# Optimization experiments

Hardware: AMD Instinct MI355X
Metric: run time of the kernel (lower is better)

## Reference

```python
import jax, jax.numpy as jnp
import numpy as np

B, L, DIN, D, H, NL, DFF = 4, 1024, 64, 512, 8, 3, 2048
DH = D // H
N_RBF = 8
LARGE_NEG, CLAMP = 10000.0, 20.0


def layernorm(x, g, b, eps=1e-5):
    m = x.mean(-1, keepdims=True)
    v = x.var(-1, keepdims=True)
    return (x - m) * jax.lax.rsqrt(v + eps) * g + b


def sinusoidal_pe(length, d):
    pos = np.arange(length, dtype=np.float32)[:, None]
    div = np.exp(np.arange(0, d, 2, dtype=np.float32) * (-np.log(10000.0) / d))
    pe = np.zeros((length, d), dtype=np.float32)
    pe[:, 0::2] = np.sin(pos * div)
    pe[:, 1::2] = np.cos(pos * div)
    return jnp.asarray(pe)


def rbf(v):
    centers = jnp.linspace(0.0, 1.0, N_RBF)
    widths = jnp.full((N_RBF,), 0.2)
    diff = (v[..., None] - centers) / (widths + 1e-6)
    return jnp.exp(-0.5 * diff * diff)


def setup_inputs() -> dict:
    key = jax.random.key(0)
    ks = jax.random.split(key, 40)
    g = lambda k, shape: (jax.random.normal(k, shape) * 0.02).astype(jnp.float32)
    feat_dim = D + 2 + 2 * N_RBF  # base PE + raw(2) + 2 RBFs
    inp = {
        "x": jax.random.normal(ks[0], (B, L, DIN), jnp.float32),
        "lengths": jax.random.randint(ks[1], (B,), L // 2, L + 1),
        "input_delay": jax.random.uniform(ks[2], (B,), jnp.float32),
        "c_local": jax.random.uniform(ks[3], (B, L), jnp.float32).at[:, 0].set(0.0),
        "c_sink": jax.random.uniform(ks[4], (B, L), jnp.float32),
        # input projection
        "in_w": g(ks[5], (D, DIN)), "in_b": jnp.zeros((D,)),
        # delay encoder: Linear(1,D) -> GELU -> Linear(D,D) -> LN
        "de_w1": g(ks[6], (D, 1)), "de_b1": jnp.zeros((D,)),
        "de_w2": g(ks[7], (D, D)), "de_b2": jnp.zeros((D,)),
        "de_ln_g": jnp.ones((D,)), "de_ln_b": jnp.zeros((D,)),
        # corr positional encoding
        "cpe_w": g(ks[8], (D, feat_dim)), "cpe_b": jnp.zeros((D,)),
        "cpe_ln_g": jnp.ones((D,)), "cpe_ln_b": jnp.zeros((D,)),
        "gain": jnp.float32(0.5),
        # bias params
        "alpha": jnp.float32(10.0), "beta": jnp.float32(10.0),
        "floor": jnp.float32(0.1), "gamma": jnp.float32(0.7),
        # per-layer stacks
        "inproj_w": g(ks[9], (NL, 3 * D, D)), "inproj_b": jnp.zeros((NL, 3 * D)),
        "outproj_w": g(ks[10], (NL, D, D)), "outproj_b": jnp.zeros((NL, D)),
        "ln1_g": jnp.ones((NL, D)), "ln1_b": jnp.zeros((NL, D)),
        "ln2_g": jnp.ones((NL, D)), "ln2_b": jnp.zeros((NL, D)),
        "ff_w1": g(ks[11], (NL, DFF, D)), "ff_b1": jnp.zeros((NL, DFF)),
        "ff_w2": g(ks[12], (NL, D, DFF)), "ff_b2": jnp.zeros((NL, D)),
        "out_ln_g": jnp.ones((D,)), "out_ln_b": jnp.zeros((D,)),
    }
    return inp


def _forward(x, input_delay, c_local, c_sink, in_w, in_b, de_w1, de_b1, de_w2, de_b2,
             de_ln_g, de_ln_b, cpe_w, cpe_b, cpe_ln_g, cpe_ln_b, gain, alpha, beta,
             floor, gamma, inproj_w, inproj_b, outproj_w, outproj_b, ln1_g, ln1_b,
             ln2_g, ln2_b, ff_w1, ff_b1, ff_w2, ff_b2, out_ln_g, out_ln_b, lengths):
    Bc, Lc, _ = x.shape
    mask = jnp.arange(Lc)[None, :] >= lengths[:, None]          # [B,L] True=pad

    # input projection
    h = x @ in_w.T + in_b

    # delay feature encoder
    e = input_delay[:, None] @ de_w1.T + de_b1
    e = jax.nn.gelu(e, approximate=False) @ de_w2.T + de_b2
    e = layernorm(e, de_ln_g, de_ln_b)
    h = h + e[:, None, :]

    # corr positional encoding (uses clamped correlations)
    cl = jnp.clip(c_local, 0.0, 1.0)
    cs = jnp.clip(c_sink, 0.0, 1.0)
    pe_base = jnp.broadcast_to(sinusoidal_pe(Lc, D)[None], (Bc, Lc, D))
    z = jnp.concatenate([pe_base, jnp.stack([cl, cs], -1), rbf(cl), rbf(cs)], axis=-1)
    pe = layernorm(z @ cpe_w.T + cpe_b, cpe_ln_g, cpe_ln_b)
    pe = gain * pe
    pe = jnp.where(mask[..., None], 0.0, pe)
    h = h + pe

    # neighbor-correlation attention bias [B,1,L,L] (identical across layers/heads)
    idx = jnp.arange(Lc)
    neigh = jnp.abs(idx[None, :] - idx[:, None]) == 1           # [L,L]
    c_edge = jnp.zeros((Bc, Lc, Lc), x.dtype)
    c_edge = c_edge.at[:, 1:, :-1].set(jnp.broadcast_to(c_local[:, 1:, None], (Bc, Lc - 1, Lc - 1)))
    c_edge = c_edge.at[:, :-1, 1:].set(jnp.broadcast_to(c_local[:, None, 1:], (Bc, Lc - 1, Lc - 1)))
    bias = alpha * jnp.where(neigh[None], c_edge, 0.0)
    bias = jnp.where(mask[:, :, None] | mask[:, None, :], 0.0, bias)

    # sink bias (row 0 only): floor + (1-floor)*(c_sink^gamma)
    c_remap = floor + (1.0 - floor) * jnp.power(cs + 1e-6, gamma)
    sink_row = beta * jnp.where(mask, 0.0, c_remap)             # [B,L]
    attn_bias = bias[:, None].at[:, :, 0, :].add(sink_row[:, None, :])  # [B,1,L,L]

    pad = mask[:, None, None, :].astype(x.dtype)                # [B,1,1,L]
    scale = 1.0 / (DH ** 0.5)

    for i in range(NL):
        hn = layernorm(h, ln1_g[i], ln1_b[i])
        qkv = hn @ inproj_w[i].T + inproj_b[i]                  # [B,L,3D]
        q, k, v = jnp.split(qkv, 3, axis=-1)
        q = q.reshape(Bc, Lc, H, DH).transpose(0, 2, 1, 3)      # [B,H,L,d]
        k = k.reshape(Bc, Lc, H, DH).transpose(0, 2, 1, 3)
        v = v.reshape(Bc, Lc, H, DH).transpose(0, 2, 1, 3)
        scores = jnp.einsum('bhqd,bhkd->bhqk', q, k) * scale + attn_bias
        scores = scores - LARGE_NEG * pad
        scores = scores - scores.max(axis=-1, keepdims=True)
        scores = jnp.clip(scores, -CLAMP, CLAMP)
        attn = jax.nn.softmax(scores, axis=-1)
        o = jnp.einsum('bhqk,bhkd->bhqd', attn, v)
        o = o.transpose(0, 2, 1, 3).reshape(Bc, Lc, D)
        h = h + (o @ outproj_w[i].T + outproj_b[i])
        hn2 = layernorm(h, ln2_g[i], ln2_b[i])
        ff = jax.nn.gelu(hn2 @ ff_w1[i].T + ff_b1[i], approximate=False)
        h = h + (ff @ ff_w2[i].T + ff_b2[i])

    return layernorm(h, out_ln_g, out_ln_b)


def reference(x, lengths, input_delay, c_local, c_sink, in_w, in_b, de_w1, de_b1,
              de_w2, de_b2, de_ln_g, de_ln_b, cpe_w, cpe_b, cpe_ln_g, cpe_ln_b, gain,
              alpha, beta, floor, gamma, inproj_w, inproj_b, outproj_w, outproj_b,
              ln1_g, ln1_b, ln2_g, ln2_b, ff_w1, ff_b1, ff_w2, ff_b2, out_ln_g, out_ln_b):
    return _forward(x, input_delay, c_local, c_sink, in_w, in_b, de_w1, de_b1, de_w2,
                    de_b2, de_ln_g, de_ln_b, cpe_w, cpe_b, cpe_ln_g, cpe_ln_b, gain,
                    alpha, beta, floor, gamma, inproj_w, inproj_b, outproj_w,
                    outproj_b, ln1_g, ln1_b, ln2_g, ln2_b, ff_w1, ff_b1, ff_w2, ff_b2,
                    out_ln_g, out_ln_b, lengths)
```

## Files before the change

kernel.cpp:

```cpp
#include <hip/hip_runtime.h>
#include <math.h>

#define BB 4
#define LL 1024
#define DIN 64
#define DD 512
#define HH 8
#define DH 64
#define NLAYER 3
#define DFF 2048
#define FEAT 530
#define FEATP 576
#define MM 4096

typedef float f32x4 __attribute__((ext_vector_type(4)));
typedef short s16x8 __attribute__((ext_vector_type(8)));

__device__ __forceinline__ unsigned short f2bf(float f) {
    unsigned int u = __float_as_uint(f);
    u += 0x7fffu + ((u >> 16) & 1u);
    return (unsigned short)(u >> 16);
}
__device__ __forceinline__ float bf2f(unsigned short u) {
    return __uint_as_float(((unsigned int)u) << 16);
}
__device__ __forceinline__ float gelu_exact(float x) {
    return 0.5f * x * (1.0f + erff(x * 0.7071067811865475f));
}
__device__ __forceinline__ float wave_reduce_sum(float v) {
    #pragma unroll
    for (int o = 32; o; o >>= 1) v += __shfl_down(v, o);
    return v;
}
__device__ __forceinline__ void gload16(const unsigned short* g, unsigned short* l) {
    __builtin_amdgcn_global_load_lds(
        (const __attribute__((address_space(1))) unsigned int*)g,
        (__attribute__((address_space(3))) unsigned int*)l, 16, 0, 0);
}
__device__ __forceinline__ void cvt16(const float* src, unsigned short* dst) {
    float4 f0 = ((const float4*)src)[0];
    float4 f1 = ((const float4*)src)[1];
    float4 f2 = ((const float4*)src)[2];
    float4 f3 = ((const float4*)src)[3];
    ushort4 o0, o1, o2, o3;
    o0.x = f2bf(f0.x); o0.y = f2bf(f0.y); o0.z = f2bf(f0.z); o0.w = f2bf(f0.w);
    o1.x = f2bf(f1.x); o1.y = f2bf(f1.y); o1.z = f2bf(f1.z); o1.w = f2bf(f1.w);
    o2.x = f2bf(f2.x); o2.y = f2bf(f2.y); o2.z = f2bf(f2.z); o2.w = f2bf(f2.w);
    o3.x = f2bf(f3.x); o3.y = f2bf(f3.y); o3.z = f2bf(f3.z); o3.w = f2bf(f3.w);
    ((ushort4*)dst)[0] = o0;
    ((ushort4*)dst)[1] = o1;
    ((ushort4*)dst)[2] = o2;
    ((ushort4*)dst)[3] = o3;
}

__global__ __launch_bounds__(256) void prologue_kernel(
    const float* __restrict__ c_local, const float* __restrict__ c_sink,
    const int* __restrict__ lengths,
    const float* __restrict__ beta_p, const float* __restrict__ floor_p,
    const float* __restrict__ gamma_p,
    unsigned short* __restrict__ Z, float* __restrict__ srow,
    const float* __restrict__ x, const float* __restrict__ in_w,
    const float* __restrict__ cpe_w,
    unsigned short* __restrict__ x_bf, unsigned short* __restrict__ w_in,
    unsigned short* __restrict__ w_cpe,
    const float* __restrict__ delay, const float* __restrict__ de_w1, const float* __restrict__ de_b1,
    const float* __restrict__ de_w2, const float* __restrict__ de_b2,
    float* __restrict__ e_pre)
{
    int blk = blockIdx.x;
    int t = threadIdx.x;

    if (blk < LL) {
        int l = blk;
        for (int d = t; d < DD; d += 256) {
            int i = d >> 1;
            float dv = expf((float)(2 * i) * (-0.017988946135618352f));
            float ang = (float)l * dv;
            unsigned short pv = f2bf((d & 1) ? cosf(ang) : sinf(ang));
            #pragma unroll
            for (int bb = 0; bb < 4; ++bb)
                Z[(size_t)(bb * LL + l) * FEATP + d] = pv;
        }
        {
            int bb = t >> 6, j = t & 63;
            float cl = c_local[(size_t)bb * LL + l]; cl = fminf(fmaxf(cl, 0.f), 1.f);
            float cs = c_sink [(size_t)bb * LL + l]; cs = fminf(fmaxf(cs, 0.f), 1.f);
            float v = 0.f;
            if (j == 0) v = cl;
            else if (j == 1) v = cs;
            else if (j < 10)  { float c = (float)(j - 2) * (1.0f / 7.0f);  float df = (cl - c) / 0.200001f; v = expf(-0.5f * df * df); }
            else if (j < 18)  { float c = (float)(j - 10) * (1.0f / 7.0f); float df = (cs - c) / 0.200001f; v = expf(-0.5f * df * df); }
            Z[(size_t)(bb * LL + l) * FEATP + 512 + j] = (j < 18) ? f2bf(v) : 0;
            if (j == 32) {
                float sv = (*beta_p) * ((*floor_p) + (1.f - (*floor_p)) * powf(cs + 1e-6f, *gamma_p));
                srow[bb * LL + l] = (l < lengths[bb]) ? sv : 0.f;
            }
        }
    } else if (blk < LL + 256) {
        const int N0s = MM * DIN;
        const int N1s = N0s + 512 * 64;
        const int NCHs = N1s / 16;
        int vb = blk - LL;
        for (int c = vb * 256 + t; c < NCHs; c += 256 * 256) {
            int i = c * 16;
            if (i < N0s) cvt16(x + i, x_bf + i);
            else         cvt16(in_w + (i - N0s), w_in + (i - N0s));
        }
        for (int j = vb * 256 + t; j < 512 * FEATP; j += 256 * 256) {
            int r = j / FEATP, c2 = j - r * FEATP;
            w_cpe[j] = (c2 < FEAT) ? f2bf(cpe_w[(size_t)r * FEAT + c2]) : 0;
        }
    } else {
        __shared__ float g1[DD];
        int idx = blk - (LL + 256);
        int b  = idx >> 4;
        int r0 = (idx & 15) * 32;
        float d0 = delay[b];
        g1[t]       = gelu_exact(d0 * de_w1[t]       + de_b1[t]);
        g1[t + 256] = gelu_exact(d0 * de_w1[t + 256] + de_b1[t + 256]);
        __syncthreads();
        int r = t >> 3, c = t & 7;
        const float* wr = de_w2 + (size_t)(r0 + r) * DD + c * 64;
        const float* gc = g1 + c * 64;
        float s = 0.f;
        #pragma unroll
        for (int j = 0; j < 64; j += 4) {
            float4 a4 = *(const float4*)(wr + j);
            s += a4.x * gc[j] + a4.y * gc[j+1] + a4.z * gc[j+2] + a4.w * gc[j+3];
        }
        s += __shfl_xor(s, 1);
        s += __shfl_xor(s, 2);
        s += __shfl_xor(s, 4);
        if (c == 0) e_pre[(size_t)b * DD + r0 + r] = s + de_b2[r0 + r];
    }
}

template<int BM, int BN, int FM, int FN, int WGN>
__device__ __forceinline__ void gemm_body(
    const unsigned short* __restrict__ A, const unsigned short* __restrict__ W,
    const float* __restrict__ bias, const unsigned short* __restrict__ residb,
    float* __restrict__ outf, unsigned short* __restrict__ outb,
    int M, int N, int K, int mode, int bm, int bn,
    unsigned short* As, unsigned short* Ws)
{
    int t = threadIdx.x;
    int lane = t & 63, wid = t >> 6;
    int wr = wid / WGN, wc = wid % WGN;
    int l15 = lane & 15, lg = lane >> 4;
    int sr = lane >> 3;
    int sc = ((lane & 7) ^ sr) * 8;
    int ph0 = (lg ^ (l15 & 7)) * 8;
    int ph1 = ((lg + 4) ^ (l15 & 7)) * 8;

    f32x4 acc[FM][FN] = {};
    int nk = K >> 6;

    auto stage = [&](int buf, int ks) {
        int kb = ks * 64;
        #pragma unroll
        for (int i = 0; i < BM / 32; ++i) {
            int row = wid * (BM / 4) + i * 8 + sr;
            gload16(A + (size_t)(bm + row) * K + kb + sc, &As[(size_t)buf * BM * 64 + (wid * (BM / 4) + i * 8) * 64]);
        }
        #pragma unroll
        for (int i = 0; i < BN / 32; ++i) {
            int row = wid * (BN / 4) + i * 8 + sr;
            gload16(W + (size_t)(bn + row) * K + kb + sc, &Ws[(size_t)buf * BN * 64 + (wid * (BN / 4) + i * 8) * 64]);
        }
    };

    stage(0, 0);
    __syncthreads();

    int cur = 0;
    for (int ks = 0; ks < nk; ++ks) {
        if (ks + 1 < nk) stage(cur ^ 1, ks + 1);
        s16x8 af0[FM], af1[FM], wf0[FN], wf1[FN];
        #pragma unroll
        for (int mi = 0; mi < FM; ++mi) {
            int row = wr * FM * 16 + mi * 16 + l15;
            af0[mi] = *(const s16x8*)&As[(size_t)cur * BM * 64 + row * 64 + ph0];
            af1[mi] = *(const s16x8*)&As[(size_t)cur * BM * 64 + row * 64 + ph1];
        }
        #pragma unroll
        for (int ni = 0; ni < FN; ++ni) {
            int row = wc * FN * 16 + ni * 16 + l15;
            wf0[ni] = *(const s16x8*)&Ws[(size_t)cur * BN * 64 + row * 64 + ph0];
            wf1[ni] = *(const s16x8*)&Ws[(size_t)cur * BN * 64 + row * 64 + ph1];
        }
        #pragma unroll
        for (int mi = 0; mi < FM; ++mi)
            #pragma unroll
            for (int ni = 0; ni < FN; ++ni) {
                acc[mi][ni] = __builtin_amdgcn_mfma_f32_16x16x32_bf16(af0[mi], wf0[ni], acc[mi][ni], 0, 0, 0);
                acc[mi][ni] = __builtin_amdgcn_mfma_f32_16x16x32_bf16(af1[mi], wf1[ni], acc[mi][ni], 0, 0, 0);
            }
        __syncthreads();
        cur ^= 1;
    }

    int rbase = (lane >> 4) * 4;
    #pragma unroll
    for (int mi = 0; mi < FM; ++mi) {
        #pragma unroll
        for (int ni = 0; ni < FN; ++ni) {
            int n = bn + wc * FN * 16 + ni * 16 + l15;
            float bzc = (mode == 4) ? 0.f : bias[n];
            #pragma unroll
            for (int r2 = 0; r2 < 4; ++r2) {
                int m = bm + wr * FM * 16 + mi * 16 + rbase + r2;
                float v = acc[mi][ni][r2] + ((mode == 4) ? bias[m] : bzc);
                size_t o = (size_t)m * N + n;
                if (mode == 0)      outf[o] = v;
                else if (mode == 1) outb[o] = f2bf(v);
                else if (mode == 2) outb[o] = f2bf(v + bf2f(residb[o]));
                else if (mode == 3) outb[o] = f2bf(gelu_exact(v));
                else                outb[o] = f2bf(v);
            }
        }
    }
}

template<int BM, int BN, int FM, int FN, int WGN, int MODE>
__global__ __launch_bounds__(256) void gemm_t(
    const unsigned short* __restrict__ A, const unsigned short* __restrict__ W,
    const float* __restrict__ bias, const unsigned short* __restrict__ residb,
    float* __restrict__ outf, unsigned short* __restrict__ outb,
    int M, int N, int K)
{
    __shared__ __align__(16) unsigned short As[2 * BM * 64];
    __shared__ __align__(16) unsigned short Ws[2 * BN * 64];
    gemm_body<BM, BN, FM, FN, WGN>(A, W, bias, residb, outf, outb, M, N, K, MODE,
                                   blockIdx.y * BM, blockIdx.x * BN, As, Ws);
}

__global__ __launch_bounds__(256) void gemm_pre_dual(
    const unsigned short* __restrict__ x_bf, const unsigned short* __restrict__ w_in,
    const float* __restrict__ in_b, unsigned short* __restrict__ h,
    const unsigned short* __restrict__ Zb, const unsigned short* __restrict__ w_cpe,
    const float* __restrict__ cpe_b, float* __restrict__ cpe_pre,
    const float* __restrict__ inproj_w, const float* __restrict__ outproj_w,
    const float* __restrict__ ff_w1, const float* __restrict__ ff_w2,
    unsigned short* __restrict__ w_inproj, unsigned short* __restrict__ w_outproj,
    unsigned short* __restrict__ w_ff1, unsigned short* __restrict__ w_ff2)
{
    __shared__ __align__(16) unsigned short As[2 * 64 * 64];
    __shared__ __align__(16) unsigned short Ws[2 * 64 * 64];
    int id = blockIdx.x;
    if (id < 512) {
        gemm_body<64, 64, 2, 2, 2>(x_bf, w_in, in_b, nullptr, nullptr, h,
                                   MM, DD, DIN, 1, (id >> 3) * 64, (id & 7) * 64, As, Ws);
    } else if (id < 1024) {
        id -= 512;
        gemm_body<64, 64, 2, 2, 2>(Zb, w_cpe, cpe_b, nullptr, cpe_pre, nullptr,
                                   MM, DD, FEATP, 0, (id >> 3) * 64, (id & 7) * 64, As, Ws);
    } else {
        const int B0 = 3 * 1536 * 512;
        const int B1 = B0 + 3 * 512 * 512;
        const int B2 = B1 + 3 * 2048 * 512;
        const int B3 = B2 + 3 * 512 * 2048;
        const int NCH = B3 / 16;
        int vb = id - 1024;
        int t = threadIdx.x;
        for (int c = vb * 256 + t; c < NCH; c += 1024 * 256) {
            int i = c * 16;
            if (i < B0)      cvt16(inproj_w + i,         w_inproj + i);
            else if (i < B1) cvt16(outproj_w + (i - B0), w_outproj + (i - B0));
            else if (i < B2) cvt16(ff_w1 + (i - B1),     w_ff1 + (i - B1));
            else             cvt16(ff_w2 + (i - B2),     w_ff2 + (i - B2));
        }
    }
}

__global__ __launch_bounds__(256) void gemm_qkv_dual(
    const unsigned short* __restrict__ act1,
    const unsigned short* __restrict__ wqk, const float* __restrict__ qk_bias,
    unsigned short* __restrict__ qkb,
    const unsigned short* __restrict__ wv, const float* __restrict__ v_bias,
    unsigned short* __restrict__ vtb)
{
    __shared__ __align__(16) unsigned short As[2 * 64 * 64];
    __shared__ __align__(16) unsigned short Ws[2 * 64 * 64];
    int id = blockIdx.x;
    if (id < 1024) {
        gemm_body<64, 64, 2, 2, 2>(act1, wqk, qk_bias, nullptr, nullptr, qkb,
                                   MM, 1024, DD, 1, (id >> 4) * 64, (id & 15) * 64, As, Ws);
    } else {
        id -= 1024;
        gemm_body<64, 64, 2, 2, 2>(wv, act1, v_bias, nullptr, nullptr, vtb,
                                   DD, MM, DD, 4, (id >> 6) * 64, (id & 63) * 64, As, Ws);
    }
}

#define SK 72
#define SPB 72
__global__ __launch_bounds__(256) void attn_mfma(
    const unsigned short* __restrict__ qk, const unsigned short* __restrict__ Vt,
    const float* __restrict__ c_local, const float* __restrict__ srow,
    const int* __restrict__ lengths,
    const float* __restrict__ alpha_p,
    unsigned short* __restrict__ o)
{
    __shared__ __align__(16) unsigned short Ks[2][64 * SK];
    __shared__ __align__(16) unsigned short Vts[2][64 * SK];
    __shared__ __align__(16) unsigned short Psb[64 * SPB];

    int id = blockIdx.x;
    int q0 = (id & 15) * 64;
    int hh = (id >> 4) & 7;
    int b  = id >> 7;

    int t  = threadIdx.x;
    int lane = t & 63, w = t >> 6;
    int l15 = lane & 15, lg = lane >> 4;
    int len = lengths[b];
    int nt = (len + 63) >> 6;
    int kt0 = q0 >> 6;
    bool sink_blk = (q0 == 0);
    const float alpha = *alpha_p;

    const unsigned short* qrow = qk + (size_t)(b * LL + q0 + w * 16 + l15) * 1024 + hh * DH;
    s16x8 qf0 = *(const s16x8*)(qrow + lg * 8);
    s16x8 qf1 = *(const s16x8*)(qrow + 32 + lg * 8);
    #pragma unroll
    for (int j = 0; j < 8; ++j) {
        qf0[j] = (short)f2bf(bf2f((unsigned short)qf0[j]) * 0.125f);
        qf1[j] = (short)f2bf(bf2f((unsigned short)qf1[j]) * 0.125f);
    }

    float cm1[4], cp1[4];
    #pragma unroll
    for (int r2 = 0; r2 < 4; ++r2) {
        int qi = q0 + w * 16 + lg * 4 + r2;
        cm1[r2] = 0.f; cp1[r2] = 0.f;
        if (qi >= 1 && qi < len) {
            int src = (qi == 1 || qi == LL - 1) ? qi : qi - 1;
            cm1[r2] = alpha * c_local[(size_t)b * LL + src];
        }
        if (qi + 1 < LL && qi < len)
            cp1[r2] = alpha * c_local[(size_t)b * LL + qi + 1];
    }
    bool need_sink = (sink_blk && w == 0 && lg == 0);

    float m_run[4], l_run[4];
    f32x4 accO[4] = {};
    #pragma unroll
    for (int r2 = 0; r2 < 4; ++r2) { m_run[r2] = -1e30f; l_run[r2] = 0.f; }

    int sr = t >> 3, sc8 = (t & 7) * 8;
    const unsigned short* kbase = qk + (size_t)(b * LL) * 1024 + 512 + hh * DH;
    const unsigned short* vbase = Vt + (size_t)(hh * DH) * MM + b * LL;

    uint4 pk0 = *(const uint4*)(kbase + (size_t)sr * 1024 + sc8);
    uint4 pk1 = *(const uint4*)(kbase + (size_t)(sr + 32) * 1024 + sc8);
    uint4 pv0 = *(const uint4*)(vbase + (size_t)sr * MM + sc8);
    uint4 pv1 = *(const uint4*)(vbase + (size_t)(sr + 32) * MM + sc8);
    *(uint4*)&Ks[0][sr * SK + sc8]         = pk0;
    *(uint4*)&Ks[0][(sr + 32) * SK + sc8]  = pk1;
    *(uint4*)&Vts[0][sr * SK + sc8]        = pv0;
    *(uint4*)&Vts[0][(sr + 32) * SK + sc8] = pv1;
    __syncthreads();

    int cur = 0;
    for (int kt = 0; kt < nt; ++kt) {
        int k0 = kt * 64;
        bool pre = (kt + 1 < nt);
        if (pre) {
            int kn = k0 + 64;
            pk0 = *(const uint4*)(kbase + (size_t)(kn + sr) * 1024 + sc8);
            pk1 = *(const uint4*)(kbase + (size_t)(kn + sr + 32) * 1024 + sc8);
            pv0 = *(const uint4*)(vbase + (size_t)sr * MM + kn + sc8);
            pv1 = *(const uint4*)(vbase + (size_t)(sr + 32) * MM + kn + sc8);
        }

        f32x4 accS[4] = {};
        #pragma unroll
        for (int ct = 0; ct < 4; ++ct) {
            s16x8 kf0 = *(const s16x8*)&Ks[cur][(ct * 16 + l15) * SK + lg * 8];
            s16x8 kf1 = *(const s16x8*)&Ks[cur][(ct * 16 + l15) * SK + 32 + lg * 8];
            accS[ct] = __builtin_amdgcn_mfma_f32_16x16x32_bf16(qf0, kf0, accS[ct], 0, 0, 0);
            accS[ct] = __builtin_amdgcn_mfma_f32_16x16x32_bf16(qf1, kf1, accS[ct], 0, 0, 0);
        }

        float m4[4] = { -1e30f, -1e30f, -1e30f, -1e30f };
        bool slow = sink_blk || (kt >= kt0 - 1 && kt <= kt0 + 1) || (k0 + 64 > len);
        if (!slow) {
            #pragma unroll
            for (int ct = 0; ct < 4; ++ct)
                #pragma unroll
                for (int r2 = 0; r2 < 4; ++r2)
                    m4[r2] = fmaxf(m4[r2], accS[ct][r2]);
        } else if (k0 + 64 <= len) {
            #pragma unroll
            for (int ct = 0; ct < 4; ++ct) {
                int k = k0 + ct * 16 + l15;
                float sink_ct = need_sink ? srow[(size_t)b * LL + k] : 0.f;
                #pragma unroll
                for (int r2 = 0; r2 < 4; ++r2) {
                    int qi = q0 + w * 16 + lg * 4 + r2;
                    float v = accS[ct][r2];
                    if (k == qi - 1) v += cm1[r2];
                    else if (k == qi + 1) v += cp1[r2];
                    if (r2 == 0) v += sink_ct;
                    accS[ct][r2] = v;
                    m4[r2] = fmaxf(m4[r2], v);
                }
            }
        } else {
            #pragma unroll
            for (int ct = 0; ct < 4; ++ct) {
                int k = k0 + ct * 16 + l15;
                bool maskk = (k >= len);
                float sink_ct = need_sink ? srow[(size_t)b * LL + k] : 0.f;
                #pragma unroll
                for (int r2 = 0; r2 < 4; ++r2) {
                    int qi = q0 + w * 16 + lg * 4 + r2;
                    float v = accS[ct][r2];
                    if (k == qi - 1) v += cm1[r2];
                    else if (k == qi + 1 && !maskk) v += cp1[r2];
                    if (r2 == 0) v += sink_ct;
                    if (maskk) v -= 10000.f;
                    accS[ct][r2] = v;
                    m4[r2] = fmaxf(m4[r2], v);
                }
            }
        }

        #pragma unroll
        for (int r2 = 0; r2 < 4; ++r2) {
            #pragma unroll
            for (int msk = 1; msk < 16; msk <<= 1) m4[r2] = fmaxf(m4[r2], __shfl_xor(m4[r2], msk));
            float mnew = fmaxf(m_run[r2], m4[r2]);
            float scl = __expf(m_run[r2] - mnew);
            m_run[r2] = mnew;
            float rowsum = 0.f;
            #pragma unroll
            for (int ct = 0; ct < 4; ++ct) {
                float p = __expf(accS[ct][r2] - mnew);
                rowsum += p;
                Psb[(w * 16 + lg * 4 + r2) * SPB + ct * 16 + l15] = f2bf(p);
            }
            #pragma unroll
            for (int msk = 1; msk < 16; msk <<= 1) rowsum += __shfl_xor(rowsum, msk);
            l_run[r2] = l_run[r2] * scl + rowsum;
            #pragma unroll
            for (int dt = 0; dt < 4; ++dt) accO[dt][r2] *= scl;
        }

        #pragma unroll
        for (int kk = 0; kk < 2; ++kk) {
            s16x8 pf = *(const s16x8*)&Psb[(w * 16 + l15) * SPB + kk * 32 + lg * 8];
            #pragma unroll
            for (int dt = 0; dt < 4; ++dt) {
                s16x8 vf = *(const s16x8*)&Vts[cur][(dt * 16 + l15) * SK + kk * 32 + lg * 8];
                accO[dt] = __builtin_amdgcn_mfma_f32_16x16x32_bf16(pf, vf, accO[dt], 0, 0, 0);
            }
        }

        if (pre) {
            int nxt = cur ^ 1;
            *(uint4*)&Ks[nxt][sr * SK + sc8]         = pk0;
            *(uint4*)&Ks[nxt][(sr + 32) * SK + sc8]  = pk1;
            *(uint4*)&Vts[nxt][sr * SK + sc8]        = pv0;
            *(uint4*)&Vts[nxt][(sr + 32) * SK + sc8] = pv1;
        }
        __syncthreads();
        cur ^= 1;
    }

    #pragma unroll
    for (int r2 = 0; r2 < 4; ++r2) {
        float inv = 1.f / l_run[r2];
        int qi = q0 + w * 16 + lg * 4 + r2;
        #pragma unroll
        for (int dt = 0; dt < 4; ++dt)
            o[(size_t)(b * LL + qi) * DD + hh * DH + dt * 16 + l15] = f2bf(accO[dt][r2] * inv);
    }
}

__global__ __launch_bounds__(256) void embed_ep_kernel(
    const float* __restrict__ cpe_pre, const float* __restrict__ e_pre,
    const int* __restrict__ lengths,
    const float* __restrict__ cpe_g, const float* __restrict__ cpe_lb,
    const float* __restrict__ de_lng, const float* __restrict__ de_lnb,
    const float* __restrict__ gain_p, unsigned short* __restrict__ h)
{
    int row = blockIdx.x;
    int b = row >> 10, l = row & 1023;
    int t = threadIdx.x;
    __shared__ float red[32];
    const float* cp = cpe_pre + (size_t)row * DD;
    float v0 = cp[t], v1 = cp[t + 256];
    float e0 = e_pre[(size_t)b * DD + t], e1 = e_pre[(size_t)b * DD + t + 256];
    float s  = v0 + v1, ss  = v0 * v0 + v1 * v1;
    float s2 = e0 + e1, ss2 = e0 * e0 + e1 * e1;
    float rs  = wave_reduce_sum(s),  rss  = wave_reduce_sum(ss);
    float rs2 = wave_reduce_sum(s2), rss2 = wave_reduce_sum(ss2);
    int lane = t & 63, w = t >> 6;
    if (lane == 0) { red[w] = rs; red[8 + w] = rss; red[16 + w] = rs2; red[24 + w] = rss2; }
    __syncthreads();
    float mean = 0.f, msq = 0.f, mean_e = 0.f, msq_e = 0.f;
    #pragma unroll
    for (int i = 0; i < 4; ++i) {
        mean += red[i]; msq += red[8 + i];
        mean_e += red[16 + i]; msq_e += red[24 + i];
    }
    mean *= (1.0f / DD); msq *= (1.0f / DD);
    mean_e *= (1.0f / DD); msq_e *= (1.0f / DD);
    float rstd   = rsqrtf(msq - mean * mean + 1e-5f);
    float rstd_e = rsqrtf(msq_e - mean_e * mean_e + 1e-5f);
    float eln0 = (e0 - mean_e) * rstd_e * de_lng[t]       + de_lnb[t];
    float eln1 = (e1 - mean_e) * rstd_e * de_lng[t + 256] + de_lnb[t + 256];
    bool maskp = (l >= lengths[b]);
    float gain = *gain_p;
    float pe0 = maskp ? 0.f : gain * ((v0 - mean) * rstd * cpe_g[t] + cpe_lb[t]);
    float pe1 = maskp ? 0.f : gain * ((v1 - mean) * rstd * cpe_g[t + 256] + cpe_lb[t + 256]);
    size_t o0 = (size_t)row * DD + t;
    size_t o1 = (size_t)row * DD + t + 256;
    h[o0] = f2bf(bf2f(h[o0]) + eln0 + pe0);
    h[o1] = f2bf(bf2f(h[o1]) + eln1 + pe1);
}

__global__ __launch_bounds__(256) void ln_kernel(
    const unsigned short* __restrict__ in, float* __restrict__ out,
    const float* __restrict__ g, const float* __restrict__ bta)
{
    int row = blockIdx.x; int t = threadIdx.x;
    __shared__ float red[16];
    const unsigned short* xr = in + (size_t)row * DD;
    ushort2 u = ((const ushort2*)xr)[t];
    float vx = bf2f(u.x), vy = bf2f(u.y);
    float s = vx + vy, ss = vx * vx + vy * vy;
    float rs = wave_reduce_sum(s), rss = wave_reduce_sum(ss);
    int lane = t & 63, w = t >> 6;
    if (lane == 0) { red[w] = rs; red[8 + w] = rss; }
    __syncthreads();
    float mean = 0.f, msq = 0.f;
    #pragma unroll
    for (int i = 0; i < 4; ++i) { mean += red[i]; msq += red[8 + i]; }
    mean *= (1.0f / DD); msq *= (1.0f / DD);
    float rstd = rsqrtf(msq - mean * mean + 1e-5f);
    float2 gg = ((const float2*)g)[t], bb = ((const float2*)bta)[t];
    float2 o;
    o.x = (vx - mean) * rstd * gg.x + bb.x;
    o.y = (vy - mean) * rstd * gg.y + bb.y;
    ((float2*)(out + (size_t)row * DD))[t] = o;
}

__global__ __launch_bounds__(256) void ln_bf16_kernel(
    const unsigned short* __restrict__ in, unsigned short* __restrict__ out,
    const float* __restrict__ g, const float* __restrict__ bta)
{
    int row = blockIdx.x; int t = threadIdx.x;
    __shared__ float red[16];
    const unsigned short* xr = in + (size_t)row * DD;
    ushort2 u = ((const ushort2*)xr)[t];
    float vx = bf2f(u.x), vy = bf2f(u.y);
    float s = vx + vy, ss = vx * vx + vy * vy;
    float rs = wave_reduce_sum(s), rss = wave_reduce_sum(ss);
    int lane = t & 63, w = t >> 6;
    if (lane == 0) { red[w] = rs; red[8 + w] = rss; }
    __syncthreads();
    float mean = 0.f, msq = 0.f;
    #pragma unroll
    for (int i = 0; i < 4; ++i) { mean += red[i]; msq += red[8 + i]; }
    mean *= (1.0f / DD); msq *= (1.0f / DD);
    float rstd = rsqrtf(msq - mean * mean + 1e-5f);
    float2 gg = ((const float2*)g)[t], bb = ((const float2*)bta)[t];
    ushort2 o;
    o.x = f2bf((vx - mean) * rstd * gg.x + bb.x);
    o.y = f2bf((vy - mean) * rstd * gg.y + bb.y);
    ((ushort2*)(out + (size_t)row * DD))[t] = o;
}

extern "C" void kernel_launch(void* const* d_in, const int* in_sizes, int n_in,
                              void* d_out, int out_size, void* d_ws, size_t ws_size,
                              hipStream_t stream)
{
    const float* x          = (const float*)d_in[0];
    const int*   lengths    = (const int*)  d_in[1];
    const float* input_delay= (const float*)d_in[2];
    const float* c_local    = (const float*)d_in[3];
    const float* c_sink     = (const float*)d_in[4];
    const float* in_w       = (const float*)d_in[5];
    const float* in_b       = (const float*)d_in[6];
    const float* de_w1      = (const float*)d_in[7];
    const float* de_b1      = (const float*)d_in[8];
    const float* de_w2      = (const float*)d_in[9];
    const float* de_b2      = (const float*)d_in[10];
    const float* de_ln_g    = (const float*)d_in[11];
    const float* de_ln_b    = (const float*)d_in[12];
    const float* cpe_w      = (const float*)d_in[13];
    const float* cpe_b      = (const float*)d_in[14];
    const float* cpe_ln_g   = (const float*)d_in[15];
    const float* cpe_ln_b   = (const float*)d_in[16];
    const float* gain       = (const float*)d_in[17];
    const float* alpha      = (const float*)d_in[18];
    const float* beta       = (const float*)d_in[19];
    const float* floorp     = (const float*)d_in[20];
    const float* gammap     = (const float*)d_in[21];
    const float* inproj_w   = (const float*)d_in[22];
    const float* inproj_b   = (const float*)d_in[23];
    const float* outproj_w  = (const float*)d_in[24];
    const float* outproj_b  = (const float*)d_in[25];
    const float* ln1_g      = (const float*)d_in[26];
    const float* ln1_b      = (const float*)d_in[27];
    const float* ln2_g      = (const float*)d_in[28];
    const float* ln2_b      = (const float*)d_in[29];
    const float* ff_w1      = (const float*)d_in[30];
    const float* ff_b1      = (const float*)d_in[31];
    const float* ff_w2      = (const float*)d_in[32];
    const float* ff_b2      = (const float*)d_in[33];
    const float* out_ln_g   = (const float*)d_in[34];
    const float* out_ln_b   = (const float*)d_in[35];

    char* base = (char*)d_ws;
    unsigned short* h    = (unsigned short*)base;
    unsigned short* act1 = (unsigned short*)(base + 8u*1024*1024);
    char* bigb          = base + 12u*1024*1024;
    unsigned short* qkb  = (unsigned short*)bigb;
    unsigned short* vtb  = (unsigned short*)(bigb + 12u*1024*1024);
    unsigned short* ffb  = (unsigned short*)bigb;
    unsigned short* Zb   = (unsigned short*)bigb;
    unsigned short* x_bf = (unsigned short*)(bigb + 5u*1024*1024);
    float* cpe_pre       = (float*)(bigb + 8u*1024*1024);
    unsigned short* w_inproj  = (unsigned short*)(base + 28u*1024*1024);
    unsigned short* w_outproj = w_inproj  + (size_t)3*1536*512;
    unsigned short* w_ff1     = w_outproj + (size_t)3*512*512;
    unsigned short* w_ff2     = w_ff1     + (size_t)3*2048*512;
    unsigned short* w_in      = w_ff2     + (size_t)3*512*2048;
    unsigned short* w_cpe     = w_in      + (size_t)512*64;
    float* e_pre              = (float*)(w_cpe + (size_t)512*FEATP);
    float* srow               = e_pre + (size_t)BB*DD;

    prologue_kernel<<<LL + 256 + 64, 256, 0, stream>>>(
        c_local, c_sink, lengths, beta, floorp, gammap, Zb, srow,
        x, in_w, cpe_w, x_bf, w_in, w_cpe,
        input_delay, de_w1, de_b1, de_w2, de_b2, e_pre);

    gemm_pre_dual<<<2048, 256, 0, stream>>>(x_bf, w_in, in_b, h, Zb, w_cpe, cpe_b, cpe_pre,
                                            inproj_w, outproj_w, ff_w1, ff_w2,
                                            w_inproj, w_outproj, w_ff1, w_ff2);
    embed_ep_kernel<<<MM, 256, 0, stream>>>(cpe_pre, e_pre, lengths, cpe_ln_g, cpe_ln_b,
                                            de_ln_g, de_ln_b, gain, h);

    for (int i = 0; i < NLAYER; ++i) {
        const unsigned short* wqk = w_inproj + (size_t)i * 1536 * 512;
        const unsigned short* wv  = wqk + (size_t)1024 * 512;
        ln_bf16_kernel<<<MM, 256, 0, stream>>>(h, act1, ln1_g + (size_t)i * DD, ln1_b + (size_t)i * DD);
        gemm_qkv_dual<<<1536, 256, 0, stream>>>(act1, wqk, inproj_b + (size_t)i * 1536,
                                                qkb, wv, inproj_b + (size_t)i * 1536 + 1024, vtb);
        attn_mfma<<<512, 256, 0, stream>>>(qkb, vtb, c_local, srow, lengths, alpha, act1);
        gemm_t<64, 64, 2, 2, 2, 2><<<dim3(DD / 64, MM / 64), 256, 0, stream>>>(
            act1, w_outproj + (size_t)i * 512 * 512, outproj_b + (size_t)i * DD,
            h, nullptr, h, MM, DD, DD);
        ln_bf16_kernel<<<MM, 256, 0, stream>>>(h, act1, ln2_g + (size_t)i * DD, ln2_b + (size_t)i * DD);
        gemm_t<128, 128, 4, 4, 2, 3><<<dim3(DFF / 128, MM / 128), 256, 0, stream>>>(
            act1, w_ff1 + (size_t)i * 2048 * 512, ff_b1 + (size_t)i * DFF,
            nullptr, nullptr, ffb, MM, DFF, DD);
        gemm_t<64, 64, 2, 2, 2, 2><<<dim3(DD / 64, MM / 64), 256, 0, stream>>>(
            ffb, w_ff2 + (size_t)i * 512 * 2048, ff_b2 + (size_t)i * DD,
            h, nullptr, h, MM, DD, DFF);
    }
    ln_kernel<<<MM, 256, 0, stream>>>(h, (float*)d_out, out_ln_g, out_ln_b);
}
```

Baseline: 389.7 us.

## Fold LayerNorm into following GEMMs via weight-folded gamma and epilogue row stats

Removes the per-layer ln_bf16 kernels by folding LN gamma into the bf16 weights, precomputing per-column sums of the folded weights and of beta·W, and applying mean and rstd in the GEMM epilogue. Row sum and sum-of-squares are accumulated by atomics in the residual GEMM epilogues and in the embed kernel. This drops two launches and two activation round trips per layer. In exchange the GEMMs now run on un-normalized bf16 h, and variance is computed as E[x²]−mean², which may lose precision. It also adds atomics and zero-initialisation of the stats buffers.

```diff
diff --git a/kernel.cpp b/kernel.cpp
--- a/kernel.cpp
+++ b/kernel.cpp
@@ -52,7 +52,23 @@
     ((ushort4*)dst)[2] = o2;
     ((ushort4*)dst)[3] = o3;
 }
-
+__device__ __forceinline__ void cvt16_fold(const float* src, const float* g, const float* bt,
+                                           unsigned short* dst, float& pc1, float& pc2) {
+    #pragma unroll
+    for (int q = 0; q < 4; ++q) {
+        float4 w4 = ((const float4*)src)[q];
+        float4 g4 = ((const float4*)g)[q];
+        float4 b4 = ((const float4*)bt)[q];
+        float fw0 = w4.x * g4.x, fw1 = w4.y * g4.y, fw2 = w4.z * g4.z, fw3 = w4.w * g4.w;
+        ushort4 o;
+        o.x = f2bf(fw0); o.y = f2bf(fw1); o.z = f2bf(fw2); o.w = f2bf(fw3);
+        ((ushort4*)dst)[q] = o;
+        pc1 += (fw0 + fw1) + (fw2 + fw3);
+        pc2 += (b4.x * w4.x + b4.y * w4.y) + (b4.z * w4.z + b4.w * w4.w);
+    }
+}
+
+#define NSTAT_FLOATS (7 * MM * 2 + 2 * 3 * 1536 + 2 * 3 * 2048)
 __global__ __launch_bounds__(256) void prologue_kernel(
     const float* __restrict__ c_local, const float* __restrict__ c_sink,
     const int* __restrict__ lengths,
@@ -65,7 +81,7 @@
     unsigned short* __restrict__ w_cpe,
     const float* __restrict__ delay, const float* __restrict__ de_w1, const float* __restrict__ de_b1,
     const float* __restrict__ de_w2, const float* __restrict__ de_b2,
-    float* __restrict__ e_pre)
+    float* __restrict__ e_pre, float* __restrict__ zbuf)
 {
     int blk = blockIdx.x;
     int t = threadIdx.x;
@@ -110,6 +126,8 @@
             int r = j / FEATP, c2 = j - r * FEATP;
             w_cpe[j] = (c2 < FEAT) ? f2bf(cpe_w[(size_t)r * FEAT + c2]) : 0;
         }
+        for (int j = vb * 256 + t; j < NSTAT_FLOATS; j += 256 * 256)
+            zbuf[j] = 0.f;
     } else {
         __shared__ float g1[DD];
         int idx = blk - (LL + 256);
@@ -141,7 +159,9 @@
     const float* __restrict__ bias, const unsigned short* __restrict__ residb,
     float* __restrict__ outf, unsigned short* __restrict__ outb,
     int M, int N, int K, int mode, int bm, int bn,
-    unsigned short* As, unsigned short* Ws)
+    unsigned short* As, unsigned short* Ws,
+    const float* __restrict__ c1, const float* __restrict__ c2,
+    const float* __restrict__ statsIn, float* __restrict__ statsOut)
 {
     int t = threadIdx.x;
     int lane = t & 63, wid = t >> 6;
@@ -200,22 +220,87 @@
     }
 
     int rbase = (lane >> 4) * 4;
-    #pragma unroll
-    for (int mi = 0; mi < FM; ++mi) {
+    if (mode == 5 || mode == 7) {
+        #pragma unroll
+        for (int mi = 0; mi < FM; ++mi) {
+            #pragma unroll
+            for (int r2 = 0; r2 < 4; ++r2) {
+                int m = bm + wr * FM * 16 + mi * 16 + rbase + r2;
+                float sm = statsIn[2 * m], sq = statsIn[2 * m + 1];
+                float mean = sm * (1.0f / DD);
+                float rstd = rsqrtf(sq * (1.0f / DD) - mean * mean + 1e-5f);
+                float rm = rstd * mean;
+                #pragma unroll
+                for (int ni = 0; ni < FN; ++ni) {
+                    int n = bn + wc * FN * 16 + ni * 16 + l15;
+                    float v = rstd * acc[mi][ni][r2] - rm * c1[n] + c2[n] + bias[n];
+                    if (mode == 7) v = gelu_exact(v);
+                    outb[(size_t)m * N + n] = f2bf(v);
+                }
+            }
+        }
+    } else if (mode == 6) {
         #pragma unroll
         for (int ni = 0; ni < FN; ++ni) {
             int n = bn + wc * FN * 16 + ni * 16 + l15;
-            float bzc = (mode == 4) ? 0.f : bias[n];
-            #pragma unroll
-            for (int r2 = 0; r2 < 4; ++r2) {
-                int m = bm + wr * FM * 16 + mi * 16 + rbase + r2;
-                float v = acc[mi][ni][r2] + ((mode == 4) ? bias[m] : bzc);
-                size_t o = (size_t)m * N + n;
-                if (mode == 0)      outf[o] = v;
-                else if (mode == 1) outb[o] = f2bf(v);
-                else if (mode == 2) outb[o] = f2bf(v + bf2f(residb[o]));
-                else if (mode == 3) outb[o] = f2bf(gelu_exact(v));
-                else                outb[o] = f2bf(v);
+            float sm = statsIn[2 * n], sq = statsIn[2 * n + 1];
+            float mean = sm * (1.0f / DD);
+            float rstd = rsqrtf(sq * (1.0f / DD) - mean * mean + 1e-5f);
+            float rm = rstd * mean;
+            #pragma unroll
+            for (int mi = 0; mi < FM; ++mi) {
+                #pragma unroll
+                for (int r2 = 0; r2 < 4; ++r2) {
+                    int m = bm + wr * FM * 16 + mi * 16 + rbase + r2;
+                    float v = rstd * acc[mi][ni][r2] - rm * c1[m] + c2[m] + bias[m];
+                    outb[(size_t)m * N + n] = f2bf(v);
+                }
+            }
+        }
+    } else {
+        float rsum[FM][4], rsq[FM][4];
+        #pragma unroll
+        for (int mi = 0; mi < FM; ++mi)
+            #pragma unroll
+            for (int r2 = 0; r2 < 4; ++r2) { rsum[mi][r2] = 0.f; rsq[mi][r2] = 0.f; }
+        #pragma unroll
+        for (int mi = 0; mi < FM; ++mi) {
+            #pragma unroll
+            for (int ni = 0; ni < FN; ++ni) {
+                int n = bn + wc * FN * 16 + ni * 16 + l15;
+                float bzc = (mode == 4) ? 0.f : bias[n];
+                #pragma unroll
+                for (int r2 = 0; r2 < 4; ++r2) {
+                    int m = bm + wr * FM * 16 + mi * 16 + rbase + r2;
+                    float v = acc[mi][ni][r2] + ((mode == 4) ? bias[m] : bzc);
+                    size_t o = (size_t)m * N + n;
+                    if (mode == 0)      outf[o] = v;
+                    else if (mode == 1) outb[o] = f2bf(v);
+                    else if (mode == 2) {
+                        v += bf2f(residb[o]);
+                        outb[o] = f2bf(v);
+                        rsum[mi][r2] += v; rsq[mi][r2] += v * v;
+                    }
+                    else                outb[o] = f2bf(v);
+                }
+            }
+        }
+        if (mode == 2 && statsOut) {
+            #pragma unroll
+            for (int mi = 0; mi < FM; ++mi) {
+                #pragma unroll
+                for (int r2 = 0; r2 < 4; ++r2) {
+                    float a = rsum[mi][r2], q = rsq[mi][r2];
+                    a += __shfl_xor(a, 1); q += __shfl_xor(q, 1);
+                    a += __shfl_xor(a, 2); q += __shfl_xor(q, 2);
+                    a += __shfl_xor(a, 4); q += __shfl_xor(q, 4);
+                    a += __shfl_xor(a, 8); q += __shfl_xor(q, 8);
+                    if (l15 == 0) {
+                        int m = bm + wr * FM * 16 + mi * 16 + rbase + r2;
+                        atomicAdd(&statsOut[2 * m], a);
+                        atomicAdd(&statsOut[2 * m + 1], q);
+                    }
+                }
             }
         }
     }
@@ -226,12 +311,15 @@
     const unsigned short* __restrict__ A, const unsigned short* __restrict__ W,
     const float* __restrict__ bias, const unsigned short* __restrict__ residb,
     float* __restrict__ outf, unsigned short* __restrict__ outb,
-    int M, int N, int K)
+    int M, int N, int K,
+    const float* __restrict__ c1, const float* __restrict__ c2,
+    const float* __restrict__ statsIn, float* __restrict__ statsOut)
 {
     __shared__ __align__(16) unsigned short As[2 * BM * 64];
     __shared__ __align__(16) unsigned short Ws[2 * BN * 64];
     gemm_body<BM, BN, FM, FN, WGN>(A, W, bias, residb, outf, outb, M, N, K, MODE,
-                                   blockIdx.y * BM, blockIdx.x * BN, As, Ws);
+                                   blockIdx.y * BM, blockIdx.x * BN, As, Ws,
+                                   c1, c2, statsIn, statsOut);
 }
 
 __global__ __launch_bounds__(256) void gemm_pre_dual(
@@ -242,18 +330,24 @@
     const float* __restrict__ inproj_w, const float* __restrict__ outproj_w,
     const float* __restrict__ ff_w1, const float* __restrict__ ff_w2,
     unsigned short* __restrict__ w_inproj, unsigned short* __restrict__ w_outproj,
-    unsigned short* __restrict__ w_ff1, unsigned short* __restrict__ w_ff2)
+    unsigned short* __restrict__ w_ff1, unsigned short* __restrict__ w_ff2,
+    const float* __restrict__ ln1_g, const float* __restrict__ ln1_b,
+    const float* __restrict__ ln2_g, const float* __restrict__ ln2_b,
+    float* __restrict__ c1_in, float* __restrict__ c2_in,
+    float* __restrict__ c1_ff, float* __restrict__ c2_ff)
 {
     __shared__ __align__(16) unsigned short As[2 * 64 * 64];
     __shared__ __align__(16) unsigned short Ws[2 * 64 * 64];
     int id = blockIdx.x;
     if (id < 512) {
         gemm_body<64, 64, 2, 2, 2>(x_bf, w_in, in_b, nullptr, nullptr, h,
-                                   MM, DD, DIN, 1, (id >> 3) * 64, (id & 7) * 64, As, Ws);
+                                   MM, DD, DIN, 1, (id >> 3) * 64, (id & 7) * 64, As, Ws,
+                                   nullptr, nullptr, nullptr, nullptr);
     } else if (id < 1024) {
         id -= 512;
         gemm_body<64, 64, 2, 2, 2>(Zb, w_cpe, cpe_b, nullptr, cpe_pre, nullptr,
-                                   MM, DD, FEATP, 0, (id >> 3) * 64, (id & 7) * 64, As, Ws);
+                                   MM, DD, FEATP, 0, (id >> 3) * 64, (id & 7) * 64, As, Ws,
+                                   nullptr, nullptr, nullptr, nullptr);
     } else {
         const int B0 = 3 * 1536 * 512;
         const int B1 = B0 + 3 * 512 * 512;
@@ -264,31 +358,54 @@
         int t = threadIdx.x;
         for (int c = vb * 256 + t; c < NCH; c += 1024 * 256) {
             int i = c * 16;
-            if (i < B0)      cvt16(inproj_w + i,         w_inproj + i);
-            else if (i < B1) cvt16(outproj_w + (i - B0), w_outproj + (i - B0));
-            else if (i < B2) cvt16(ff_w1 + (i - B1),     w_ff1 + (i - B1));
-            else             cvt16(ff_w2 + (i - B2),     w_ff2 + (i - B2));
+            if (i < B0) {
+                int L = i / (1536 * 512), rem = i - L * (1536 * 512);
+                int n = rem >> 9, k = rem & 511;
+                float pc1 = 0.f, pc2 = 0.f;
+                cvt16_fold(inproj_w + i, ln1_g + L * 512 + k, ln1_b + L * 512 + k,
+                           w_inproj + i, pc1, pc2);
+                atomicAdd(&c1_in[L * 1536 + n], pc1);
+                atomicAdd(&c2_in[L * 1536 + n], pc2);
+            } else if (i < B1) {
+                cvt16(outproj_w + (i - B0), w_outproj + (i - B0));
+            } else if (i < B2) {
+                int j = i - B1;
+                int L = j / (2048 * 512), rem = j - L * (2048 * 512);
+                int n = rem >> 9, k = rem & 511;
+                float pc1 = 0.f, pc2 = 0.f;
+                cvt16_fold(ff_w1 + j, ln2_g + L * 512 + k, ln2_b + L * 512 + k,
+                           w_ff1 + j, pc1, pc2);
+                atomicAdd(&c1_ff[L * 2048 + n], pc1);
+                atomicAdd(&c2_ff[L * 2048 + n], pc2);
+            } else {
+                cvt16(ff_w2 + (i - B2), w_ff2 + (i - B2));
+            }
         }
     }
 }
 
 __global__ __launch_bounds__(256) void gemm_qkv_dual(
-    const unsigned short* __restrict__ act1,
+    const unsigned short* __restrict__ h,
     const unsigned short* __restrict__ wqk, const float* __restrict__ qk_bias,
     unsigned short* __restrict__ qkb,
     const unsigned short* __restrict__ wv, const float* __restrict__ v_bias,
-    unsigned short* __restrict__ vtb)
+    unsigned short* __restrict__ vtb,
+    const float* __restrict__ c1q, const float* __restrict__ c2q,
+    const float* __restrict__ c1v, const float* __restrict__ c2v,
+    const float* __restrict__ stats)
 {
     __shared__ __align__(16) unsigned short As[2 * 64 * 64];
     __shared__ __align__(16) unsigned short Ws[2 * 64 * 64];
     int id = blockIdx.x;
     if (id < 1024) {
-        gemm_body<64, 64, 2, 2, 2>(act1, wqk, qk_bias, nullptr, nullptr, qkb,
-                                   MM, 1024, DD, 1, (id >> 4) * 64, (id & 15) * 64, As, Ws);
+        gemm_body<64, 64, 2, 2, 2>(h, wqk, qk_bias, nullptr, nullptr, qkb,
+                                   MM, 1024, DD, 5, (id >> 4) * 64, (id & 15) * 64, As, Ws,
+                                   c1q, c2q, stats, nullptr);
     } else {
         id -= 1024;
-        gemm_body<64, 64, 2, 2, 2>(wv, act1, v_bias, nullptr, nullptr, vtb,
-                                   DD, MM, DD, 4, (id >> 6) * 64, (id & 63) * 64, As, Ws);
+        gemm_body<64, 64, 2, 2, 2>(wv, h, v_bias, nullptr, nullptr, vtb,
+                                   DD, MM, DD, 6, (id >> 6) * 64, (id & 63) * 64, As, Ws,
+                                   c1v, c2v, stats, nullptr);
     }
 }
 
@@ -483,7 +600,8 @@
     const int* __restrict__ lengths,
     const float* __restrict__ cpe_g, const float* __restrict__ cpe_lb,
     const float* __restrict__ de_lng, const float* __restrict__ de_lnb,
-    const float* __restrict__ gain_p, unsigned short* __restrict__ h)
+    const float* __restrict__ gain_p, unsigned short* __restrict__ h,
+    float* __restrict__ stats0)
 {
     int row = blockIdx.x;
     int b = row >> 10, l = row & 1023;
@@ -517,8 +635,21 @@
     float pe1 = maskp ? 0.f : gain * ((v1 - mean) * rstd * cpe_g[t + 256] + cpe_lb[t + 256]);
     size_t o0 = (size_t)row * DD + t;
     size_t o1 = (size_t)row * DD + t + 256;
-    h[o0] = f2bf(bf2f(h[o0]) + eln0 + pe0);
-    h[o1] = f2bf(bf2f(h[o1]) + eln1 + pe1);
+    float hn0 = bf2f(h[o0]) + eln0 + pe0;
+    float hn1 = bf2f(h[o1]) + eln1 + pe1;
+    h[o0] = f2bf(hn0);
+    h[o1] = f2bf(hn1);
+    float s3 = hn0 + hn1, ss3 = hn0 * hn0 + hn1 * hn1;
+    float rs3 = wave_reduce_sum(s3), rss3 = wave_reduce_sum(ss3);
+    __syncthreads();
+    if (lane == 0) { red[w] = rs3; red[8 + w] = rss3; }
+    __syncthreads();
+    if (t == 0) {
+        float a = red[0] + red[1] + red[2] + red[3];
+        float q = red[8] + red[9] + red[10] + red[11];
+        stats0[2 * row] = a;
+        stats0[2 * row + 1] = q;
+    }
 }
 
 __global__ __launch_bounds__(256) void ln_kernel(
@@ -545,32 +676,6 @@
     o.x = (vx - mean) * rstd * gg.x + bb.x;
     o.y = (vy - mean) * rstd * gg.y + bb.y;
     ((float2*)(out + (size_t)row * DD))[t] = o;
-}
-
-__global__ __launch_bounds__(256) void ln_bf16_kernel(
-    const unsigned short* __restrict__ in, unsigned short* __restrict__ out,
-    const float* __restrict__ g, const float* __restrict__ bta)
-{
-    int row = blockIdx.x; int t = threadIdx.x;
-    __shared__ float red[16];
-    const unsigned short* xr = in + (size_t)row * DD;
-    ushort2 u = ((const ushort2*)xr)[t];
-    float vx = bf2f(u.x), vy = bf2f(u.y);
-    float s = vx + vy, ss = vx * vx + vy * vy;
-    float rs = wave_reduce_sum(s), rss = wave_reduce_sum(ss);
-    int lane = t & 63, w = t >> 6;
-    if (lane == 0) { red[w] = rs; red[8 + w] = rss; }
-    __syncthreads();
-    float mean = 0.f, msq = 0.f;
-    #pragma unroll
-    for (int i = 0; i < 4; ++i) { mean += red[i]; msq += red[8 + i]; }
-    mean *= (1.0f / DD); msq *= (1.0f / DD);
-    float rstd = rsqrtf(msq - mean * mean + 1e-5f);
-    float2 gg = ((const float2*)g)[t], bb = ((const float2*)bta)[t];
-    ushort2 o;
-    o.x = f2bf((vx - mean) * rstd * gg.x + bb.x);
-    o.y = f2bf((vy - mean) * rstd * gg.y + bb.y);
-    ((ushort2*)(out + (size_t)row * DD))[t] = o;
 }
 
 extern "C" void kernel_launch(void* const* d_in, const int* in_sizes, int n_in,
@@ -616,7 +721,7 @@
 
     char* base = (char*)d_ws;
     unsigned short* h    = (unsigned short*)base;
-    unsigned short* act1 = (unsigned short*)(base + 8u*1024*1024);
+    unsigned short* ao   = (unsigned short*)(base + 8u*1024*1024);
     char* bigb          = base + 12u*1024*1024;
     unsigned short* qkb  = (unsigned short*)bigb;
     unsigned short* vtb  = (unsigned short*)(bigb + 12u*1024*1024);
@@ -632,35 +737,51 @@
     unsigned short* w_cpe     = w_in      + (size_t)512*64;
     float* e_pre              = (float*)(w_cpe + (size_t)512*FEATP);
     float* srow               = e_pre + (size_t)BB*DD;
+    float* zbuf               = srow + (size_t)BB*LL;
+    float* stats_ln1          = zbuf;
+    float* stats_ln2          = stats_ln1 + (size_t)4 * MM * 2;
+    float* c1_in              = stats_ln2 + (size_t)3 * MM * 2;
+    float* c2_in              = c1_in + 3 * 1536;
+    float* c1_ff              = c2_in + 3 * 1536;
+    float* c2_ff              = c1_ff + 3 * 2048;
 
     prologue_kernel<<<LL + 256 + 64, 256, 0, stream>>>(
         c_local, c_sink, lengths, beta, floorp, gammap, Zb, srow,
         x, in_w, cpe_w, x_bf, w_in, w_cpe,
-        input_delay, de_w1, de_b1, de_w2, de_b2, e_pre);
+        input_delay, de_w1, de_b1, de_w2, de_b2, e_pre, zbuf);
 
     gemm_pre_dual<<<2048, 256, 0, stream>>>(x_bf, w_in, in_b, h, Zb, w_cpe, cpe_b, cpe_pre,
                                             inproj_w, outproj_w, ff_w1, ff_w2,
-                                            w_inproj, w_outproj, w_ff1, w_ff2);
+                                            w_inproj, w_outproj, w_ff1, w_ff2,
+                                            ln1_g, ln1_b, ln2_g, ln2_b,
+                                            c1_in, c2_in, c1_ff, c2_ff);
     embed_ep_kernel<<<MM, 256, 0, stream>>>(cpe_pre, e_pre, lengths, cpe_ln_g, cpe_ln_b,
-                                            de_ln_g, de_ln_b, gain, h);
+                                            de_ln_g, de_ln_b, gain, h, stats_ln1);
 
     for (int i = 0; i < NLAYER; ++i) {
         const unsigned short* wqk = w_inproj + (size_t)i * 1536 * 512;
         const unsigned short* wv  = wqk + (size_t)1024 * 512;
-        ln_bf16_kernel<<<MM, 256, 0, stream>>>(h, act1, ln1_g + (size_t)i * DD, ln1_b + (size_t)i * DD);
-        gemm_qkv_dual<<<1536, 256, 0, stream>>>(act1, wqk, inproj_b + (size_t)i * 1536,
-                                                qkb, wv, inproj_b + (size_t)i * 1536 + 1024, vtb);
-        attn_mfma<<<512, 256, 0, stream>>>(qkb, vtb, c_local, srow, lengths, alpha, act1);
+        float* st1  = stats_ln1 + (size_t)i * MM * 2;
+        float* st2  = stats_ln2 + (size_t)i * MM * 2;
+        float* st1n = stats_ln1 + (size_t)(i + 1) * MM * 2;
+        const float* c1L = c1_in + (size_t)i * 1536;
+        const float* c2L = c2_in + (size_t)i * 1536;
+        const float* c1F = c1_ff + (size_t)i * 2048;
+        const float* c2F = c2_ff + (size_t)i * 2048;
+
+        gemm_qkv_dual<<<1536, 256, 0, stream>>>(h, wqk, inproj_b + (size_t)i * 1536, qkb,
+                                                wv, inproj_b + (size_t)i * 1536 + 1024, vtb,
+                                                c1L, c2L, c1L + 1024, c2L + 1024, st1);
+        attn_mfma<<<512, 256, 0, stream>>>(qkb, vtb, c_local, srow, lengths, alpha, ao);
         gemm_t<64, 64, 2, 2, 2, 2><<<dim3(DD / 64, MM / 64), 256, 0, stream>>>(
-            act1, w_outproj + (size_t)i * 512 * 512, outproj_b + (size_t)i * DD,
-            h, nullptr, h, MM, DD, DD);
-        ln_bf16_kernel<<<MM, 256, 0, stream>>>(h, act1, ln2_g + (size_t)i * DD, ln2_b + (size_t)i * DD);
-        gemm_t<128, 128, 4, 4, 2, 3><<<dim3(DFF / 128, MM / 128), 256, 0, stream>>>(
-            act1, w_ff1 + (size_t)i * 2048 * 512, ff_b1 + (size_t)i * DFF,
-            nullptr, nullptr, ffb, MM, DFF, DD);
+            ao, w_outproj + (size_t)i * 512 * 512, outproj_b + (size_t)i * DD,
+            h, nullptr, h, MM, DD, DD, nullptr, nullptr, nullptr, st2);
+        gemm_t<128, 128, 4, 4, 2, 7><<<dim3(DFF / 128, MM / 128), 256, 0, stream>>>(
+            h, w_ff1 + (size_t)i * 2048 * 512, ff_b1 + (size_t)i * DFF,
+            nullptr, nullptr, ffb, MM, DFF, DD, c1F, c2F, st2, nullptr);
         gemm_t<64, 64, 2, 2, 2, 2><<<dim3(DD / 64, MM / 64), 256, 0, stream>>>(
             ffb, w_ff2 + (size_t)i * 512 * 2048, ff_b2 + (size_t)i * DD,
-            h, nullptr, h, MM, DD, DFF);
+            h, nullptr, h, MM, DD, DFF, nullptr, nullptr, nullptr, st1n);
     }
     ln_kernel<<<MM, 256, 0, stream>>>(h, (float*)d_out, out_ln_g, out_ln_b);
 }
```

After: 460.2 us. 18.1% more time.
